# Kernel optimization log

Measured on AMD Instinct MI355X. Metric: run time of the kernel, lower is better.

Reference implementation:

```python
import jax, jax.numpy as jnp
import numpy as np

EPS_PD = 1e-6      # torch.nn.PairwiseDistance default eps (added to the difference)
EPS_NORM = 1e-12   # F.normalize default eps

B, D, C = 1024, 512, 256  # batch, in_features, out_features


def _l2_normalize(x, axis):
    n = jnp.linalg.norm(x, axis=axis, keepdims=True)
    return x / jnp.maximum(n, EPS_NORM)


def _pairwise_dist(a, b):
    # Faithful to torch PairwiseDistance(p=2) with the unsqueeze(2)/t().unsqueeze(0)
    # broadcast trick: norm over the feature dim of (a[:, :, None] - b.T[None, :, :] + eps).
    # a: [N, D], b: [M, D] -> [N, M]
    diff = a[:, :, None] - b.T[None, :, :] + EPS_PD  # [N, D, M]
    return jnp.sqrt(jnp.sum(diff * diff, axis=1))


def setup_inputs() -> dict:
    key = jax.random.key(0)
    k1, k2, k3 = jax.random.split(key, 3)
    return {
        "features": jax.random.normal(k1, (B, D), dtype=jnp.float32),
        "weights": jax.random.normal(k2, (C, D), dtype=jnp.float32),          # nn.init.normal_(0,1)
        "distance_scale": jax.random.normal(k3, (1,), dtype=jnp.float32),
        "use_distance_scale": 1,
    }


def reference(features, weights, distance_scale, use_distance_scale):
    f = _l2_normalize(features, axis=1)   # [B, D]
    w = _l2_normalize(weights, axis=1)    # [C, D]
    distances = _pairwise_dist(f, w)          # [B, C]
    distances_protoc = _pairwise_dist(w, w)   # [C, C]
    logits = distances - distances_protoc.sum() * 0.1
    if use_distance_scale:
        return -logits * jnp.abs(distance_scale)
    return -logits
```

## Files before the change

kernel.cpp:

```cpp
#include <hip/hip_runtime.h>
#include <math.h>

#define DIMS 512
#define BATCH 1024
#define CLS 256
#define ROWS (BATCH + CLS)

#define EPS_PD 1e-6f
#define DEPS2 (512.0f * 1e-6f * 1e-6f)
#define EPS_NORM 1e-12f

typedef short bf16x8 __attribute__((ext_vector_type(8)));
typedef float f32x4 __attribute__((ext_vector_type(4)));

__device__ __forceinline__ float waveReduceSum(float v) {
#pragma unroll
  for (int off = 32; off > 0; off >>= 1)
    v += __shfl_xor(v, off, 64);
  return v;
}

__device__ __forceinline__ unsigned short f2bf(float x) {
  unsigned int u = __float_as_uint(x);
  u += 0x7fffu + ((u >> 16) & 1u);
  return (unsigned short)(u >> 16);
}

__global__ __launch_bounds__(64) void k_norm(
    const float* __restrict__ feat, const float* __restrict__ wt,
    unsigned short* __restrict__ fnw, float* __restrict__ Srow) {
  const int r = blockIdx.x;
  const int lane = threadIdx.x;
  const float* src = (r < BATCH) ? (feat + (size_t)r * DIMS)
                                 : (wt + (size_t)(r - BATCH) * DIMS);
  const float4* s4 = (const float4*)src;

  float4 a = s4[lane];
  float4 c = s4[lane + 64];

  float ss = a.x*a.x + a.y*a.y + a.z*a.z + a.w*a.w
           + c.x*c.x + c.y*c.y + c.z*c.z + c.w*c.w;
  float sm = a.x + a.y + a.z + a.w + c.x + c.y + c.z + c.w;
  ss = waveReduceSum(ss);
  sm = waveReduceSum(sm);
  const float rn = 1.f / fmaxf(sqrtf(ss), EPS_NORM);

  ushort4 pa, pc;
  pa.x = f2bf(a.x * rn); pa.y = f2bf(a.y * rn);
  pa.z = f2bf(a.z * rn); pa.w = f2bf(a.w * rn);
  pc.x = f2bf(c.x * rn); pc.y = f2bf(c.y * rn);
  pc.z = f2bf(c.z * rn); pc.w = f2bf(c.w * rn);

  ushort4* dst = (ushort4*)(fnw + (size_t)r * DIMS);
  dst[lane] = pa;
  dst[lane + 64] = pc;

  if (lane == 0) Srow[r] = sm * rn;
}

__global__ __launch_bounds__(64) void k_gemm(
    const unsigned short* __restrict__ fnw, float* __restrict__ dots) {
  const int lane = threadIdx.x;
  const int r0 = blockIdx.x * 32;
  const int j0 = blockIdx.y * 32;

  const int lm = lane & 15;
  const int lk = (lane >> 4) * 8;

  const unsigned short* arow0 = fnw + (size_t)(r0 + lm) * DIMS + lk;
  const unsigned short* arow1 = fnw + (size_t)(r0 + 16 + lm) * DIMS + lk;
  const unsigned short* brow0 = fnw + (size_t)(BATCH + j0 + lm) * DIMS + lk;
  const unsigned short* brow1 = fnw + (size_t)(BATCH + j0 + 16 + lm) * DIMS + lk;

  f32x4 acc00 = {0.f,0.f,0.f,0.f}, acc01 = {0.f,0.f,0.f,0.f};
  f32x4 acc10 = {0.f,0.f,0.f,0.f}, acc11 = {0.f,0.f,0.f,0.f};

#pragma unroll
  for (int k0 = 0; k0 < DIMS; k0 += 32) {
    const bf16x8 a0 = *(const bf16x8*)(arow0 + k0);
    const bf16x8 a1 = *(const bf16x8*)(arow1 + k0);
    const bf16x8 b0 = *(const bf16x8*)(brow0 + k0);
    const bf16x8 b1 = *(const bf16x8*)(brow1 + k0);
    acc00 = __builtin_amdgcn_mfma_f32_16x16x32_bf16(a0, b0, acc00, 0, 0, 0);
    acc01 = __builtin_amdgcn_mfma_f32_16x16x32_bf16(a0, b1, acc01, 0, 0, 0);
    acc10 = __builtin_amdgcn_mfma_f32_16x16x32_bf16(a1, b0, acc10, 0, 0, 0);
    acc11 = __builtin_amdgcn_mfma_f32_16x16x32_bf16(a1, b1, acc11, 0, 0, 0);
  }

  const int crow = (lane >> 4) * 4;
  const int ccol = lane & 15;
#pragma unroll
  for (int q = 0; q < 4; ++q) {
    dots[(size_t)(r0 + crow + q) * CLS + (j0 + ccol)]           = acc00[q];
    dots[(size_t)(r0 + crow + q) * CLS + (j0 + 16 + ccol)]      = acc01[q];
    dots[(size_t)(r0 + 16 + crow + q) * CLS + (j0 + ccol)]      = acc10[q];
    dots[(size_t)(r0 + 16 + crow + q) * CLS + (j0 + 16 + ccol)] = acc11[q];
  }
}

__global__ __launch_bounds__(256) void k_red(
    const float* __restrict__ dots, const float* __restrict__ Srow,
    float* __restrict__ partial) {
  const int b = blockIdx.x;
  const int t = threadIdx.x;
  const int g = b * 1024 + t * 4;
  const int i = g >> 8;
  const int j = g & 255;

  const float4 d4 = *(const float4*)(dots + (size_t)BATCH * CLS + g);
  const float swi = Srow[BATCH + i];
  const float4 swj = *(const float4*)(Srow + BATCH + j);

  float s = 0.f;
  const float dot[4] = {d4.x, d4.y, d4.z, d4.w};
  const float sw[4] = {swj.x, swj.y, swj.z, swj.w};
#pragma unroll
  for (int e = 0; e < 4; ++e) {
    float dist;
    if (i == j + e) {
      dist = sqrtf(DEPS2);
    } else {
      const float d2 = 2.f - 2.f * dot[e] + 2.f * EPS_PD * (swi - sw[e]) + DEPS2;
      dist = sqrtf(fmaxf(d2, 0.f));
    }
    s += dist;
  }

  __shared__ float red[4];
  float ws = waveReduceSum(s);
  if ((t & 63) == 0) red[t >> 6] = ws;
  __syncthreads();
  if (t == 0) partial[b] = red[0] + red[1] + red[2] + red[3];
}

__global__ __launch_bounds__(256) void k_epi(
    const float* __restrict__ dots, const float* __restrict__ Srow,
    const float* __restrict__ partial, const float* __restrict__ dscale,
    const int* __restrict__ use_ds, float* __restrict__ out) {
  const int t = threadIdx.x;

  __shared__ float sS;
  if (t < 64) {
    float v = partial[t];
    v = waveReduceSum(v);
    if (t == 0) sS = v;
  }
  __syncthreads();
  const float Ssc = 0.1f * sS;
  const float sc = (use_ds[0] != 0) ? fabsf(dscale[0]) : 1.0f;

  const int g = (blockIdx.x * 256 + t) * 4;
  const int i = g >> 8;
  const int j = g & 255;

  const float4 d4 = *(const float4*)(dots + g);
  const float sfi = Srow[i];
  const float4 swj = *(const float4*)(Srow + BATCH + j);

  const float dot[4] = {d4.x, d4.y, d4.z, d4.w};
  const float sw[4] = {swj.x, swj.y, swj.z, swj.w};
  float4 o;
  float* op = (float*)&o;
#pragma unroll
  for (int e = 0; e < 4; ++e) {
    const float d2 = 2.f - 2.f * dot[e] + 2.f * EPS_PD * (sfi - sw[e]) + DEPS2;
    const float dist = sqrtf(fmaxf(d2, 0.f));
    op[e] = (Ssc - dist) * sc;
  }
  *(float4*)(out + g) = o;
}

extern "C" void kernel_launch(void* const* d_in, const int* in_sizes, int n_in,
                              void* d_out, int out_size, void* d_ws, size_t ws_size,
                              hipStream_t stream) {
  const float* feat = (const float*)d_in[0];
  const float* wt   = (const float*)d_in[1];
  const float* ds   = (const float*)d_in[2];
  const int*   use  = (const int*)d_in[3];
  float* out = (float*)d_out;

  unsigned short* fnw = (unsigned short*)d_ws;
  float* fbase   = (float*)((char*)d_ws + (size_t)ROWS * DIMS * 2);
  float* Srow    = fbase;
  float* partial = fbase + ROWS;
  float* dots    = fbase + ROWS + 64;

  k_norm<<<ROWS, 64, 0, stream>>>(feat, wt, fnw, Srow);
  k_gemm<<<dim3(ROWS / 32, CLS / 32), 64, 0, stream>>>(fnw, dots);
  k_red<<<64, 256, 0, stream>>>(dots, Srow, partial);
  k_epi<<<256, 256, 0, stream>>>(dots, Srow, partial, ds, use, out);
}
```

Before: 20.77 us.

## Fuse distance epilogues into MFMA GEMM kernels and drop dots buffer

Result: slower. 21.42 us (+3.1%).

```diff
diff --git a/kernel.cpp b/kernel.cpp
--- a/kernel.cpp
+++ b/kernel.cpp
@@ -26,11 +26,11 @@
   return (unsigned short)(u >> 16);
 }
 
-__global__ __launch_bounds__(64) void k_norm(
+__global__ __launch_bounds__(256) void k_norm(
     const float* __restrict__ feat, const float* __restrict__ wt,
     unsigned short* __restrict__ fnw, float* __restrict__ Srow) {
-  const int r = blockIdx.x;
-  const int lane = threadIdx.x;
+  const int r = blockIdx.x * 4 + (threadIdx.x >> 6);
+  const int lane = threadIdx.x & 63;
   const float* src = (r < BATCH) ? (feat + (size_t)r * DIMS)
                                  : (wt + (size_t)(r - BATCH) * DIMS);
   const float4* s4 = (const float4*)src;
@@ -58,17 +58,18 @@
   if (lane == 0) Srow[r] = sm * rn;
 }
 
-__global__ __launch_bounds__(64) void k_gemm(
-    const unsigned short* __restrict__ fnw, float* __restrict__ dots) {
+__global__ __launch_bounds__(64) void k_protoc(
+    const unsigned short* __restrict__ fnw, const float* __restrict__ Srow,
+    float* __restrict__ partial) {
   const int lane = threadIdx.x;
-  const int r0 = blockIdx.x * 32;
-  const int j0 = blockIdx.y * 32;
+  const int i0 = blockIdx.y * 32;
+  const int j0 = blockIdx.x * 32;
 
   const int lm = lane & 15;
   const int lk = (lane >> 4) * 8;
 
-  const unsigned short* arow0 = fnw + (size_t)(r0 + lm) * DIMS + lk;
-  const unsigned short* arow1 = fnw + (size_t)(r0 + 16 + lm) * DIMS + lk;
+  const unsigned short* arow0 = fnw + (size_t)(BATCH + i0 + lm) * DIMS + lk;
+  const unsigned short* arow1 = fnw + (size_t)(BATCH + i0 + 16 + lm) * DIMS + lk;
   const unsigned short* brow0 = fnw + (size_t)(BATCH + j0 + lm) * DIMS + lk;
   const unsigned short* brow1 = fnw + (size_t)(BATCH + j0 + 16 + lm) * DIMS + lk;
 
@@ -89,85 +90,100 @@
 
   const int crow = (lane >> 4) * 4;
   const int ccol = lane & 15;
-#pragma unroll
-  for (int q = 0; q < 4; ++q) {
-    dots[(size_t)(r0 + crow + q) * CLS + (j0 + ccol)]           = acc00[q];
-    dots[(size_t)(r0 + crow + q) * CLS + (j0 + 16 + ccol)]      = acc01[q];
-    dots[(size_t)(r0 + 16 + crow + q) * CLS + (j0 + ccol)]      = acc10[q];
-    dots[(size_t)(r0 + 16 + crow + q) * CLS + (j0 + 16 + ccol)] = acc11[q];
-  }
-}
-
-__global__ __launch_bounds__(256) void k_red(
-    const float* __restrict__ dots, const float* __restrict__ Srow,
-    float* __restrict__ partial) {
-  const int b = blockIdx.x;
-  const int t = threadIdx.x;
-  const int g = b * 1024 + t * 4;
-  const int i = g >> 8;
-  const int j = g & 255;
-
-  const float4 d4 = *(const float4*)(dots + (size_t)BATCH * CLS + g);
-  const float swi = Srow[BATCH + i];
-  const float4 swj = *(const float4*)(Srow + BATCH + j);
+
+  const float swj0 = Srow[BATCH + j0 + ccol];
+  const float swj1 = Srow[BATCH + j0 + 16 + ccol];
 
   float s = 0.f;
-  const float dot[4] = {d4.x, d4.y, d4.z, d4.w};
-  const float sw[4] = {swj.x, swj.y, swj.z, swj.w};
-#pragma unroll
-  for (int e = 0; e < 4; ++e) {
-    float dist;
-    if (i == j + e) {
-      dist = sqrtf(DEPS2);
-    } else {
-      const float d2 = 2.f - 2.f * dot[e] + 2.f * EPS_PD * (swi - sw[e]) + DEPS2;
-      dist = sqrtf(fmaxf(d2, 0.f));
+  const f32x4 accs[4] = {acc00, acc01, acc10, acc11};
+#pragma unroll
+  for (int hi = 0; hi < 2; ++hi) {
+#pragma unroll
+    for (int q = 0; q < 4; ++q) {
+      const int i = i0 + hi * 16 + crow + q;
+      const float swi = Srow[BATCH + i];
+#pragma unroll
+      for (int hj = 0; hj < 2; ++hj) {
+        const int j = j0 + hj * 16 + ccol;
+        const float dot = accs[hi * 2 + hj][q];
+        const float swj = hj ? swj1 : swj0;
+        float dist;
+        if (i == j) {
+          dist = sqrtf(DEPS2);
+        } else {
+          const float d2 = 2.f - 2.f * dot + 2.f * EPS_PD * (swi - swj) + DEPS2;
+          dist = sqrtf(fmaxf(d2, 0.f));
+        }
+        s += dist;
+      }
     }
-    s += dist;
-  }
-
-  __shared__ float red[4];
-  float ws = waveReduceSum(s);
-  if ((t & 63) == 0) red[t >> 6] = ws;
-  __syncthreads();
-  if (t == 0) partial[b] = red[0] + red[1] + red[2] + red[3];
-}
-
-__global__ __launch_bounds__(256) void k_epi(
-    const float* __restrict__ dots, const float* __restrict__ Srow,
+  }
+
+  s = waveReduceSum(s);
+  if (lane == 0) partial[blockIdx.y * 8 + blockIdx.x] = s;
+}
+
+__global__ __launch_bounds__(64) void k_main(
+    const unsigned short* __restrict__ fnw, const float* __restrict__ Srow,
     const float* __restrict__ partial, const float* __restrict__ dscale,
     const int* __restrict__ use_ds, float* __restrict__ out) {
-  const int t = threadIdx.x;
-
-  __shared__ float sS;
-  if (t < 64) {
-    float v = partial[t];
-    v = waveReduceSum(v);
-    if (t == 0) sS = v;
-  }
-  __syncthreads();
-  const float Ssc = 0.1f * sS;
+  const int lane = threadIdx.x;
+  const int r0 = blockIdx.x * 32;
+  const int j0 = blockIdx.y * 32;
+
+  const float myPartial = partial[lane];
+
+  const int lm = lane & 15;
+  const int lk = (lane >> 4) * 8;
+
+  const unsigned short* arow0 = fnw + (size_t)(r0 + lm) * DIMS + lk;
+  const unsigned short* arow1 = fnw + (size_t)(r0 + 16 + lm) * DIMS + lk;
+  const unsigned short* brow0 = fnw + (size_t)(BATCH + j0 + lm) * DIMS + lk;
+  const unsigned short* brow1 = fnw + (size_t)(BATCH + j0 + 16 + lm) * DIMS + lk;
+
+  f32x4 acc00 = {0.f,0.f,0.f,0.f}, acc01 = {0.f,0.f,0.f,0.f};
+  f32x4 acc10 = {0.f,0.f,0.f,0.f}, acc11 = {0.f,0.f,0.f,0.f};
+
+#pragma unroll
+  for (int k0 = 0; k0 < DIMS; k0 += 32) {
+    const bf16x8 a0 = *(const bf16x8*)(arow0 + k0);
+    const bf16x8 a1 = *(const bf16x8*)(arow1 + k0);
+    const bf16x8 b0 = *(const bf16x8*)(brow0 + k0);
+    const bf16x8 b1 = *(const bf16x8*)(brow1 + k0);
+    acc00 = __builtin_amdgcn_mfma_f32_16x16x32_bf16(a0, b0, acc00, 0, 0, 0);
+    acc01 = __builtin_amdgcn_mfma_f32_16x16x32_bf16(a0, b1, acc01, 0, 0, 0);
+    acc10 = __builtin_amdgcn_mfma_f32_16x16x32_bf16(a1, b0, acc10, 0, 0, 0);
+    acc11 = __builtin_amdgcn_mfma_f32_16x16x32_bf16(a1, b1, acc11, 0, 0, 0);
+  }
+
+  const float S = waveReduceSum(myPartial);
+  const float Ssc = 0.1f * S;
   const float sc = (use_ds[0] != 0) ? fabsf(dscale[0]) : 1.0f;
 
-  const int g = (blockIdx.x * 256 + t) * 4;
-  const int i = g >> 8;
-  const int j = g & 255;
-
-  const float4 d4 = *(const float4*)(dots + g);
-  const float sfi = Srow[i];
-  const float4 swj = *(const float4*)(Srow + BATCH + j);
-
-  const float dot[4] = {d4.x, d4.y, d4.z, d4.w};
-  const float sw[4] = {swj.x, swj.y, swj.z, swj.w};
-  float4 o;
-  float* op = (float*)&o;
-#pragma unroll
-  for (int e = 0; e < 4; ++e) {
-    const float d2 = 2.f - 2.f * dot[e] + 2.f * EPS_PD * (sfi - sw[e]) + DEPS2;
-    const float dist = sqrtf(fmaxf(d2, 0.f));
-    op[e] = (Ssc - dist) * sc;
-  }
-  *(float4*)(out + g) = o;
+  const int crow = (lane >> 4) * 4;
+  const int ccol = lane & 15;
+
+  const float swj0 = Srow[BATCH + j0 + ccol];
+  const float swj1 = Srow[BATCH + j0 + 16 + ccol];
+
+  const f32x4 accs[4] = {acc00, acc01, acc10, acc11};
+#pragma unroll
+  for (int hi = 0; hi < 2; ++hi) {
+#pragma unroll
+    for (int q = 0; q < 4; ++q) {
+      const int i = r0 + hi * 16 + crow + q;
+      const float sfi = Srow[i];
+#pragma unroll
+      for (int hj = 0; hj < 2; ++hj) {
+        const int j = j0 + hj * 16 + ccol;
+        const float dot = accs[hi * 2 + hj][q];
+        const float swj = hj ? swj1 : swj0;
+        const float d2 = 2.f - 2.f * dot + 2.f * EPS_PD * (sfi - swj) + DEPS2;
+        const float dist = sqrtf(fmaxf(d2, 0.f));
+        out[(size_t)i * CLS + j] = (Ssc - dist) * sc;
+      }
+    }
+  }
 }
 
 extern "C" void kernel_launch(void* const* d_in, const int* in_sizes, int n_in,
@@ -183,10 +199,8 @@
   float* fbase   = (float*)((char*)d_ws + (size_t)ROWS * DIMS * 2);
   float* Srow    = fbase;
   float* partial = fbase + ROWS;
-  float* dots    = fbase + ROWS + 64;
-
-  k_norm<<<ROWS, 64, 0, stream>>>(feat, wt, fnw, Srow);
-  k_gemm<<<dim3(ROWS / 32, CLS / 32), 64, 0, stream>>>(fnw, dots);
-  k_red<<<64, 256, 0, stream>>>(dots, Srow, partial);
-  k_epi<<<256, 256, 0, stream>>>(dots, Srow, partial, ds, use, out);
-}
+
+  k_norm<<<ROWS / 4, 256, 0, stream>>>(feat, wt, fnw, Srow);
+  k_protoc<<<dim3(8, 8), 64, 0, stream>>>(fnw, Srow, partial);
+  k_main<<<dim3(32, 8), 64, 0, stream>>>(fnw, Srow, partial, ds, use, out);
+}
```
